# Performance work log

Measured on AMD Instinct MI355X. Metric: run time of the kernel, lower is better.

## Reference

```python
import jax, jax.numpy as jnp
import numpy as np
from jax import lax

B, T, H, V = 2048, 512, 256, 64


def setup_inputs() -> dict:
    key = jax.random.key(0)
    k_tok, k_emb, k_w = jax.random.split(key, 3)
    tokens = jax.random.randint(k_tok, (B, T), 0, V, dtype=jnp.int32)
    h0 = jnp.zeros((B, H), dtype=jnp.float32)
    emb = jax.random.normal(k_emb, (V, H), dtype=jnp.float32)
    # Linear(2H -> H) weight, scaled to avoid sigmoid saturation
    W = jax.random.normal(k_w, (H, 2 * H), dtype=jnp.float32) / jnp.sqrt(jnp.float32(2 * H))
    b = jnp.zeros((H,), dtype=jnp.float32)
    return {"tokens": tokens, "h0": h0, "emb": emb, "W": W, "b": b}


def reference(tokens, h0, emb, W, b):
    # Each step of the tree recursion: h = sigmoid(layer(cat(embed(tok), h)))
    # Linearized as a scan over the token sequence; dropout in eval mode (identity).
    x = emb[tokens]                 # [B, T, H] embedding lookup
    x = jnp.swapaxes(x, 0, 1)       # [T, B, H] for scan
    Wx = W[:, :H]                   # acts on embedded token
    Wh = W[:, H:]                   # acts on previous hidden
    xproj = jnp.einsum('tbh,oh->tbo', x, Wx) + b  # precompute token projections

    def step(h, xp_t):
        h_new = jax.nn.sigmoid(xp_t + h @ Wh.T)   # [B, H]
        return h_new, h_new

    _, hs = lax.scan(step, h0, xproj)
    return hs  # [T, B, H] all hidden states
```

## Files before the change

kernel.cpp:

```cpp
#include <hip/hip_runtime.h>
#include <hip/hip_bf16.h>

#define Bsz 2048
#define Tlen 512
#define Hdim 256
#define Vocab 64

typedef __attribute__((ext_vector_type(8))) __bf16 bf16x8;
typedef __attribute__((ext_vector_type(4))) float float4v;

__device__ inline unsigned short f32_bf16(float f) {
    unsigned int u = __float_as_uint(f);
    u += 0x7FFF + ((u >> 16) & 1);
    return (unsigned short)(u >> 16);
}

__device__ inline void barrier_lds() {
    asm volatile("s_waitcnt lgkmcnt(0)\n\ts_barrier" ::: "memory");
}

__global__ void build_frags(const float* __restrict__ emb,
                            const float* __restrict__ W,
                            const float* __restrict__ bias,
                            unsigned short* __restrict__ wt) {
    int idx = blockIdx.x * 256 + threadIdx.x;
    int j    = idx & 7;
    int lane = (idx >> 3) & 63;
    int fi   = idx >> 9;
    int ks   = fi % 10;
    int wnt  = fi / 10;
    int o = (wnt >> 2) * 64 + (wnt & 3) * 16 + (lane & 15);
    int k = ks * 32 + ((lane >> 4) & 3) * 8 + j;
    float val;
    if (k < Hdim) {
        val = W[o * (2 * Hdim) + Hdim + k];
    } else {
        int v = k - Hdim;
        float s = bias[o];
        for (int h = 0; h < Hdim; ++h)
            s += emb[v * Hdim + h] * W[o * (2 * Hdim) + h];
        val = s;
    }
    wt[idx] = f32_bf16(val);
}

__global__ __launch_bounds__(256, 1) void rnn_main(
        const int* __restrict__ tokens,
        const float* __restrict__ h0,
        const unsigned short* __restrict__ wt,
        float* __restrict__ out) {
    __shared__ int tok_lds[8 * 513];
    __shared__ unsigned short hb[2][8 * 264];

    const int tid  = threadIdx.x;
    const int lane = tid & 63;
    const int w    = tid >> 6;
    const int lm   = lane & 15;
    const int lg   = lane >> 4;
    const int b_base = blockIdx.x * 8;
    const int o_base = w * 64;

    const int np   = (lg >> 1) * 2;
    const int srow = (lg & 1) * 4;

    for (int e = 0; e < 16; ++e) {
        int idx = e * 256 + tid;
        int m = idx >> 9, t = idx & 511;
        tok_lds[m * 513 + t] = tokens[(b_base + m) * Tlen + t];
    }
    for (int e = 0; e < 8; ++e) {
        int idx = e * 256 + tid;
        int m = idx >> 8, c = idx & 255;
        hb[0][m * 264 + c] = f32_bf16(h0[(b_base + m) * Hdim + c]);
    }

    bf16x8 bfr[4][10];
    const bf16x8* wp = (const bf16x8*)wt;
#pragma unroll
    for (int nt = 0; nt < 4; ++nt)
#pragma unroll
        for (int ks = 0; ks < 10; ++ks)
            bfr[nt][ks] = wp[(((w * 4 + nt) * 10 + ks) * 64) + lane];

    float pv[2][4];

#pragma unroll 2
    for (int t = 0; t < Tlen; ++t) {
        const int cur = t & 1;
        const int nxt = cur ^ 1;
        barrier_lds();

        int tok = tok_lds[(lm & 7) * 513 + t];
        bf16x8 a[10];
        const unsigned short* hrow = &hb[cur][(lm & 7) * 264];
#pragma unroll
        for (int ks = 0; ks < 8; ++ks)
            a[ks] = *(const bf16x8*)(hrow + ks * 32 + lg * 8);

        if (t > 0) {
#pragma unroll
            for (int i = 0; i < 2; ++i)
#pragma unroll
                for (int r = 0; r < 4; ++r) {
                    long off = ((long)(t - 1) * Bsz + (b_base + srow + r)) * Hdim;
                    out[off + o_base + (np + i) * 16 + lm] = pv[i][r];
                }
        }

        {
            bf16x8 a8, a9;
#pragma unroll
            for (int j = 0; j < 8; ++j) {
                int v0 = lg * 8 + j;
                a8[j] = (v0 == tok)      ? (__bf16)1.0f : (__bf16)0.0f;
                a9[j] = (v0 + 32 == tok) ? (__bf16)1.0f : (__bf16)0.0f;
            }
            a[8] = a8;
            a[9] = a9;
        }

        float4v acc[4];
#pragma unroll
        for (int nt = 0; nt < 4; ++nt) {
            float4v z = {0.f, 0.f, 0.f, 0.f};
            acc[nt] = z;
        }
#pragma unroll
        for (int ks = 0; ks < 10; ++ks)
#pragma unroll
            for (int nt = 0; nt < 4; ++nt)
                acc[nt] = __builtin_amdgcn_mfma_f32_16x16x32_bf16(
                    a[ks], bfr[nt][ks], acc[nt], 0, 0, 0);

        float4v accA = (lg >= 2) ? acc[2] : acc[0];
        float4v accB = (lg >= 2) ? acc[3] : acc[1];

#pragma unroll
        for (int r = 0; r < 4; ++r) {
            float sA = 1.0f / (1.0f + __expf(-accA[r]));
            float sB = 1.0f / (1.0f + __expf(-accB[r]));
            pv[0][r] = sA;
            pv[1][r] = sB;
            int row = srow + r;
            hb[nxt][row * 264 + o_base + (np + 0) * 16 + lm] = f32_bf16(sA);
            hb[nxt][row * 264 + o_base + (np + 1) * 16 + lm] = f32_bf16(sB);
        }
    }

#pragma unroll
    for (int i = 0; i < 2; ++i)
#pragma unroll
        for (int r = 0; r < 4; ++r) {
            long off = ((long)(Tlen - 1) * Bsz + (b_base + srow + r)) * Hdim;
            out[off + o_base + (np + i) * 16 + lm] = pv[i][r];
        }
}

extern "C" void kernel_launch(void* const* d_in, const int* in_sizes, int n_in,
                              void* d_out, int out_size, void* d_ws, size_t ws_size,
                              hipStream_t stream) {
    const int*   tokens = (const int*)d_in[0];
    const float* h0     = (const float*)d_in[1];
    const float* emb    = (const float*)d_in[2];
    const float* W      = (const float*)d_in[3];
    const float* b      = (const float*)d_in[4];
    unsigned short* wt  = (unsigned short*)d_ws;

    build_frags<<<320, 256, 0, stream>>>(emb, W, b, wt);
    rnn_main<<<256, 256, 0, stream>>>(tokens, h0, wt, (float*)d_out);
}
```

Baseline: 1.329 ms.

## Split RNN step across 8 waves and shorten the serial MFMA chain per step

Doubles the block to 512 threads so each wave owns 32 output columns (2 N-tiles) instead of 64, halving the serial MFMA work and weight registers per wave. The token-projection MFMAs are moved ahead of the barrier because they do not depend on the hidden state, and the hidden-state reduction is split into two independent accumulator chains to expose more MFMA parallelism. It also uses a fast reciprocal for the sigmoid and a strength-reduced output pointer. The cost is more waves per block contending at each per-step barrier, and an extra add to combine the two accumulators.

```diff
diff --git a/kernel.cpp b/kernel.cpp
--- a/kernel.cpp
+++ b/kernel.cpp
@@ -28,8 +28,8 @@
     int lane = (idx >> 3) & 63;
     int fi   = idx >> 9;
     int ks   = fi % 10;
-    int wnt  = fi / 10;
-    int o = (wnt >> 2) * 64 + (wnt & 3) * 16 + (lane & 15);
+    int g    = fi / 10;
+    int o = g * 16 + (lane & 15);
     int k = ks * 32 + ((lane >> 4) & 3) * 8 + j;
     float val;
     if (k < Hdim) {
@@ -44,7 +44,7 @@
     wt[idx] = f32_bf16(val);
 }
 
-__global__ __launch_bounds__(256, 1) void rnn_main(
+__global__ __launch_bounds__(512, 2) void rnn_main(
         const int* __restrict__ tokens,
         const float* __restrict__ h0,
         const unsigned short* __restrict__ wt,
@@ -58,40 +58,62 @@
     const int lm   = lane & 15;
     const int lg   = lane >> 4;
     const int b_base = blockIdx.x * 8;
-    const int o_base = w * 64;
+    const int o_base = w * 32;
 
-    const int np   = (lg >> 1) * 2;
+    const int sel  = lg >> 1;
     const int srow = (lg & 1) * 4;
 
-    for (int e = 0; e < 16; ++e) {
-        int idx = e * 256 + tid;
+    for (int e = 0; e < 8; ++e) {
+        int idx = e * 512 + tid;
         int m = idx >> 9, t = idx & 511;
         tok_lds[m * 513 + t] = tokens[(b_base + m) * Tlen + t];
     }
-    for (int e = 0; e < 8; ++e) {
-        int idx = e * 256 + tid;
+    for (int e = 0; e < 4; ++e) {
+        int idx = e * 512 + tid;
         int m = idx >> 8, c = idx & 255;
         hb[0][m * 264 + c] = f32_bf16(h0[(b_base + m) * Hdim + c]);
     }
 
-    bf16x8 bfr[4][10];
+    bf16x8 bfr[2][10];
     const bf16x8* wp = (const bf16x8*)wt;
 #pragma unroll
-    for (int nt = 0; nt < 4; ++nt)
+    for (int nt = 0; nt < 2; ++nt)
 #pragma unroll
         for (int ks = 0; ks < 10; ++ks)
-            bfr[nt][ks] = wp[(((w * 4 + nt) * 10 + ks) * 64) + lane];
+            bfr[nt][ks] = wp[(((w * 2 + nt) * 10 + ks) * 64) + lane];
 
-    float pv[2][4];
+    __syncthreads();
+
+    float pv[4];
+    float* op = out + (long)(b_base + srow) * Hdim + o_base + sel * 16 + lm;
+    const long SS = (long)Bsz * Hdim;
 
 #pragma unroll 2
     for (int t = 0; t < Tlen; ++t) {
         const int cur = t & 1;
         const int nxt = cur ^ 1;
+
+        int tok = tok_lds[(lm & 7) * 513 + t];
+        bf16x8 a8, a9;
+#pragma unroll
+        for (int j = 0; j < 8; ++j) {
+            int v0 = lg * 8 + j;
+            a8[j] = (v0 == tok)      ? (__bf16)1.0f : (__bf16)0.0f;
+            a9[j] = (v0 + 32 == tok) ? (__bf16)1.0f : (__bf16)0.0f;
+        }
+        float4v ax[2];
+#pragma unroll
+        for (int nt = 0; nt < 2; ++nt) {
+            float4v z = {0.f, 0.f, 0.f, 0.f};
+            ax[nt] = __builtin_amdgcn_mfma_f32_16x16x32_bf16(
+                a8, bfr[nt][8], z, 0, 0, 0);
+            ax[nt] = __builtin_amdgcn_mfma_f32_16x16x32_bf16(
+                a9, bfr[nt][9], ax[nt], 0, 0, 0);
+        }
+
         barrier_lds();
 
-        int tok = tok_lds[(lm & 7) * 513 + t];
-        bf16x8 a[10];
+        bf16x8 a[8];
         const unsigned short* hrow = &hb[cur][(lm & 7) * 264];
 #pragma unroll
         for (int ks = 0; ks < 8; ++ks)
@@ -99,61 +121,47 @@
 
         if (t > 0) {
 #pragma unroll
-            for (int i = 0; i < 2; ++i)
-#pragma unroll
-                for (int r = 0; r < 4; ++r) {
-                    long off = ((long)(t - 1) * Bsz + (b_base + srow + r)) * Hdim;
-                    out[off + o_base + (np + i) * 16 + lm] = pv[i][r];
-                }
+            for (int r = 0; r < 4; ++r)
+                op[(long)r * Hdim] = pv[r];
+            op += SS;
         }
 
-        {
-            bf16x8 a8, a9;
+        float4v accE[2], accO[2];
 #pragma unroll
-            for (int j = 0; j < 8; ++j) {
-                int v0 = lg * 8 + j;
-                a8[j] = (v0 == tok)      ? (__bf16)1.0f : (__bf16)0.0f;
-                a9[j] = (v0 + 32 == tok) ? (__bf16)1.0f : (__bf16)0.0f;
-            }
-            a[8] = a8;
-            a[9] = a9;
+        for (int nt = 0; nt < 2; ++nt) {
+            accE[nt] = ax[nt];
+            float4v z = {0.f, 0.f, 0.f, 0.f};
+            accO[nt] = z;
+        }
+#pragma unroll
+        for (int kp = 0; kp < 4; ++kp) {
+#pragma unroll
+            for (int nt = 0; nt < 2; ++nt)
+                accE[nt] = __builtin_amdgcn_mfma_f32_16x16x32_bf16(
+                    a[2 * kp], bfr[nt][2 * kp], accE[nt], 0, 0, 0);
+#pragma unroll
+            for (int nt = 0; nt < 2; ++nt)
+                accO[nt] = __builtin_amdgcn_mfma_f32_16x16x32_bf16(
+                    a[2 * kp + 1], bfr[nt][2 * kp + 1], accO[nt], 0, 0, 0);
         }
 
-        float4v acc[4];
-#pragma unroll
-        for (int nt = 0; nt < 4; ++nt) {
-            float4v z = {0.f, 0.f, 0.f, 0.f};
-            acc[nt] = z;
-        }
-#pragma unroll
-        for (int ks = 0; ks < 10; ++ks)
-#pragma unroll
-            for (int nt = 0; nt < 4; ++nt)
-                acc[nt] = __builtin_amdgcn_mfma_f32_16x16x32_bf16(
-                    a[ks], bfr[nt][ks], acc[nt], 0, 0, 0);
+        float4v aE = sel ? accE[1] : accE[0];
+        float4v aO = sel ? accO[1] : accO[0];
 
-        float4v accA = (lg >= 2) ? acc[2] : acc[0];
-        float4v accB = (lg >= 2) ? acc[3] : acc[1];
-
+        unsigned short* hw = &hb[nxt][srow * 264 + o_base + sel * 16 + lm];
 #pragma unroll
         for (int r = 0; r < 4; ++r) {
-            float sA = 1.0f / (1.0f + __expf(-accA[r]));
-            float sB = 1.0f / (1.0f + __expf(-accB[r]));
-            pv[0][r] = sA;
-            pv[1][r] = sB;
-            int row = srow + r;
-            hb[nxt][row * 264 + o_base + (np + 0) * 16 + lm] = f32_bf16(sA);
-            hb[nxt][row * 264 + o_base + (np + 1) * 16 + lm] = f32_bf16(sB);
+            float x = aE[r] + aO[r];
+            float e = __expf(-x);
+            float s = __builtin_amdgcn_rcpf(1.0f + e);
+            pv[r] = s;
+            hw[r * 264] = f32_bf16(s);
         }
     }
 
 #pragma unroll
-    for (int i = 0; i < 2; ++i)
-#pragma unroll
-        for (int r = 0; r < 4; ++r) {
-            long off = ((long)(Tlen - 1) * Bsz + (b_base + srow + r)) * Hdim;
-            out[off + o_base + (np + i) * 16 + lm] = pv[i][r];
-        }
+    for (int r = 0; r < 4; ++r)
+        op[(long)r * Hdim] = pv[r];
 }
 
 extern "C" void kernel_launch(void* const* d_in, const int* in_sizes, int n_in,
@@ -167,5 +175,5 @@
     unsigned short* wt  = (unsigned short*)d_ws;
 
     build_frags<<<320, 256, 0, stream>>>(emb, W, b, wt);
-    rnn_main<<<256, 256, 0, stream>>>(tokens, h0, wt, (float*)d_out);
+    rnn_main<<<256, 512, 0, stream>>>(tokens, h0, wt, (float*)d_out);
 }
```

New measurement: 1.218 ms. 1.09x faster.
